# Optimization experiments

Measured on AMD Instinct MI355X. Metric: run time of the kernel, lower is better.

## Reference

```python
import jax, jax.numpy as jnp
import numpy as np

N_NODES = 100000
N_EDGES = 3200000
IN_C, HID_C, OUT_C = 128, 64, 64


def setup_inputs() -> dict:
    key = jax.random.key(0)
    k = jax.random.split(key, 6)
    x = jax.random.normal(k[0], (N_NODES, IN_C), dtype=jnp.float32)
    edge_index = jax.random.randint(k[1], (2, N_EDGES), 0, N_NODES, dtype=jnp.int64)
    edge_weight = jax.random.uniform(k[2], (N_EDGES,), dtype=jnp.float32)
    W1 = jax.random.normal(k[3], (IN_C, HID_C), dtype=jnp.float32) * (1.0 / np.sqrt(IN_C))
    b1 = jnp.zeros((HID_C,), dtype=jnp.float32)
    W2 = jax.random.normal(k[4], (HID_C, OUT_C), dtype=jnp.float32) * (1.0 / np.sqrt(HID_C))
    b2 = jnp.zeros((OUT_C,), dtype=jnp.float32)
    return {"x": x, "edge_index": edge_index, "edge_weight": edge_weight,
            "W1": W1, "b1": b1, "W2": W2, "b2": b2}


def _gcn_norm(edge_index, edge_weight, num_nodes, dtype):
    # PyG GCNConv default: add self-loops (weight 1), symmetric normalization
    loop = jnp.arange(num_nodes, dtype=edge_index.dtype)
    row = jnp.concatenate([edge_index[0], loop])  # sources
    col = jnp.concatenate([edge_index[1], loop])  # targets (aggregation dim)
    w = jnp.concatenate([edge_weight.astype(dtype), jnp.ones((num_nodes,), dtype)])
    deg = jax.ops.segment_sum(w, col, num_segments=num_nodes)
    deg_inv_sqrt = jnp.where(deg > 0, jax.lax.rsqrt(deg), jnp.zeros((), dtype))
    norm = deg_inv_sqrt[row] * w * deg_inv_sqrt[col]
    return row, col, norm


def _gcn_conv(h, row, col, norm, W, b, num_nodes):
    h = h @ W                      # [N, C_out]
    msg = h[row] * norm[:, None]   # gather over sources, scale by edge norm
    out = jax.ops.segment_sum(msg, col, num_segments=num_nodes)  # scatter-add to targets
    return out + b


def reference(x, edge_index, edge_weight, W1, b1, W2, b2):
    num_nodes = x.shape[0]
    row, col, norm = _gcn_norm(edge_index, edge_weight, num_nodes, x.dtype)
    h = _gcn_conv(x, row, col, norm, W1, b1, num_nodes)
    h = jax.nn.relu(h)
    return _gcn_conv(h, row, col, norm, W2, b2, num_nodes)
```

## Files before the change

kernel.cpp:

```cpp
#include <hip/hip_runtime.h>
#include <hip/hip_bf16.h>

#define N_NODES 100000
#define N_EDGES 3200000
#define IN_C 128
#define HID_C 64
#define OUT_C 64

#define NBUCKET 196
#define CH_GRID 1563
#define SC_EDGES 4096
#define SC_GRID 782

struct EdgeRec { int s; float v; };

__device__ __forceinline__ unsigned pack_bf16(float lo, float hi) {
    unsigned short l = __hip_bfloat16_raw(__float2bfloat16(lo)).x;
    unsigned short h = __hip_bfloat16_raw(__float2bfloat16(hi)).x;
    return ((unsigned)h << 16) | l;
}
__device__ __forceinline__ float bf_lo(unsigned u) {
    union { unsigned u; float f; } c; c.u = u << 16; return c.f;
}
__device__ __forceinline__ float bf_hi(unsigned u) {
    union { unsigned u; float f; } c; c.u = u & 0xffff0000u; return c.f;
}

__global__ __launch_bounds__(256) void coarse_hist(const int* __restrict__ tgt,
                                                   int* __restrict__ gcnt) {
    __shared__ int hist[256];
    int tid = threadIdx.x;
    hist[tid] = 0;
    __syncthreads();
    int base = blockIdx.x * 2048;
    for (int i = 0; i < 8; ++i) {
        int e = base + i * 256 + tid;
        if (e < N_EDGES) atomicAdd(&hist[tgt[e] >> 9], 1);
    }
    __syncthreads();
    if (hist[tid]) atomicAdd(&gcnt[tid], hist[tid]);
}

__global__ __launch_bounds__(256) void coarse_scan(const int* __restrict__ gcnt,
                                                   int* __restrict__ start,
                                                   int* __restrict__ cursor) {
    __shared__ int s[256];
    int tid = threadIdx.x;
    int v = gcnt[tid];
    s[tid] = v;
    __syncthreads();
    for (int off = 1; off < 256; off <<= 1) {
        int t = s[tid];
        int add = (tid >= off) ? s[tid - off] : 0;
        __syncthreads();
        s[tid] = t + add;
        __syncthreads();
    }
    int excl = s[tid] - v;
    start[tid] = excl;
    cursor[tid] = excl;
    if (tid == 255) start[256] = s[255];
}

__global__ __launch_bounds__(256) void scatter_coarse(const int* __restrict__ ei,
                                                      const float* __restrict__ ew,
                                                      int* __restrict__ gcursor,
                                                      uint2* __restrict__ tmp) {
    __shared__ int hist[256];
    __shared__ int scan[256];
    __shared__ int lcur[256];
    __shared__ int adj[256];
    __shared__ uint2 rec[SC_EDGES];
    __shared__ unsigned char bk[SC_EDGES];
    int tid = threadIdx.x;
    hist[tid] = 0;
    __syncthreads();
    int base = blockIdx.x * SC_EDGES;
    unsigned ys[16];
    float    ws[16];
    int      bs[16];
    for (int i = 0; i < 16; ++i) {
        int e = base + i * 256 + tid;
        if (e < N_EDGES) {
            int t = ei[N_EDGES + e];
            bs[i] = t >> 9;
            ys[i] = (unsigned)ei[e] | ((unsigned)(t & 511) << 17);
            ws[i] = ew[e];
            atomicAdd(&hist[bs[i]], 1);
        } else bs[i] = -1;
    }
    __syncthreads();
    int v = hist[tid];
    scan[tid] = v;
    __syncthreads();
    for (int off = 1; off < 256; off <<= 1) {
        int t = scan[tid];
        int add = (tid >= off) ? scan[tid - off] : 0;
        __syncthreads();
        scan[tid] = t + add;
        __syncthreads();
    }
    int excl = scan[tid] - v;
    int gb = (v > 0) ? atomicAdd(&gcursor[tid], v) : 0;
    lcur[tid] = excl;
    adj[tid] = gb - excl;
    __syncthreads();
    for (int i = 0; i < 16; ++i) {
        if (bs[i] >= 0) {
            int j = atomicAdd(&lcur[bs[i]], 1);
            rec[j] = make_uint2(__float_as_uint(ws[i]), ys[i]);
            bk[j] = (unsigned char)bs[i];
        }
    }
    __syncthreads();
    int count = N_EDGES - base;
    if (count > SC_EDGES) count = SC_EDGES;
    for (int j = tid; j < count; j += 256) {
        int b = bk[j];
        tmp[adj[b] + j] = rec[j];
    }
}

__global__ __launch_bounds__(512) void fine_sort(const int* __restrict__ start,
                                                 const uint2* __restrict__ tmp,
                                                 int* __restrict__ rowptr,
                                                 float* __restrict__ dis,
                                                 EdgeRec* __restrict__ ed) {
    __shared__ int   cnt[512];
    __shared__ float wdeg[512];
    __shared__ int   s[512];
    int tid = threadIdx.x;
    int nodeBase = blockIdx.x << 9;
    int bb = start[blockIdx.x];
    int be = start[blockIdx.x + 1];
    cnt[tid] = 0;
    wdeg[tid] = 0.f;
    __syncthreads();
    for (int e = bb + tid; e < be; e += 512) {
        uint2 r = tmp[e];
        int l = (r.y >> 17) & 511;
        atomicAdd(&cnt[l], 1);
        atomicAdd(&wdeg[l], __uint_as_float(r.x));
    }
    __syncthreads();
    int v = cnt[tid];
    s[tid] = v;
    __syncthreads();
    for (int off = 1; off < 512; off <<= 1) {
        int t = s[tid];
        int add = (tid >= off) ? s[tid - off] : 0;
        __syncthreads();
        s[tid] = t + add;
        __syncthreads();
    }
    int excl = s[tid] - v;
    int node = nodeBase + tid;
    if (node < N_NODES) {
        rowptr[node] = bb + excl;
        dis[node] = rsqrtf(wdeg[tid] + 1.0f);
    }
    if (node == N_NODES) rowptr[N_NODES] = N_EDGES;
    cnt[tid] = excl;
    __syncthreads();
    for (int e = bb + tid; e < be; e += 512) {
        uint2 r = tmp[e];
        int l = (r.y >> 17) & 511;
        int p = atomicAdd(&cnt[l], 1);
        EdgeRec o;
        o.s = (int)(r.y & 0x1FFFFu);
        o.v = __uint_as_float(r.x);
        ed[bb + p] = o;
    }
}

__global__ __launch_bounds__(256) void mm1_kernel(const float* __restrict__ x,
                                                  const float* __restrict__ W,
                                                  const float* __restrict__ dis,
                                                  unsigned* __restrict__ h) {
    __shared__ float xs[16][IN_C];
    __shared__ float wsm[IN_C][HID_C];
    int tid = threadIdx.x;
    {
        float4*       wd = (float4*)&wsm[0][0];
        const float4* wsrc = (const float4*)W;
        for (int i = tid; i < IN_C * HID_C / 4; i += 256) wd[i] = wsrc[i];
        float4*       xd = (float4*)&xs[0][0];
        const float4* xsrc = (const float4*)(x + (size_t)blockIdx.x * 16 * IN_C);
        for (int i = tid; i < 16 * IN_C / 4; i += 256) xd[i] = xsrc[i];
    }
    int rowBase = blockIdx.x * 16;
    __syncthreads();
    int c = tid & 63, rg = tid >> 6;
    float a0 = 0.f, a1 = 0.f, a2 = 0.f, a3 = 0.f;
    for (int k = 0; k < IN_C; ++k) {
        float wv = wsm[k][c];
        a0 += xs[rg * 4 + 0][k] * wv;
        a1 += xs[rg * 4 + 1][k] * wv;
        a2 += xs[rg * 4 + 2][k] * wv;
        a3 += xs[rg * 4 + 3][k] * wv;
    }
    a0 *= dis[rowBase + rg * 4 + 0];
    a1 *= dis[rowBase + rg * 4 + 1];
    a2 *= dis[rowBase + rg * 4 + 2];
    a3 *= dis[rowBase + rg * 4 + 3];
    float o0 = __shfl_xor(a0, 1, 64);
    float o1 = __shfl_xor(a1, 1, 64);
    float o2 = __shfl_xor(a2, 1, 64);
    float o3 = __shfl_xor(a3, 1, 64);
    if ((c & 1) == 0) {
        int ci = c >> 1;
        h[(rowBase + rg * 4 + 0) * 32 + ci] = pack_bf16(a0, o0);
        h[(rowBase + rg * 4 + 1) * 32 + ci] = pack_bf16(a1, o1);
        h[(rowBase + rg * 4 + 2) * 32 + ci] = pack_bf16(a2, o2);
        h[(rowBase + rg * 4 + 3) * 32 + ci] = pack_bf16(a3, o3);
    }
}

__global__ __launch_bounds__(256) void mm2_kernel(const float* __restrict__ a,
                                                  const float* __restrict__ W,
                                                  const float* __restrict__ dis,
                                                  unsigned* __restrict__ h) {
    __shared__ float as[16][HID_C];
    __shared__ float wsm[HID_C][OUT_C];
    int tid = threadIdx.x;
    {
        float4*       wd = (float4*)&wsm[0][0];
        const float4* wsrc = (const float4*)W;
        for (int i = tid; i < HID_C * OUT_C / 4; i += 256) wd[i] = wsrc[i];
        float4*       ad = (float4*)&as[0][0];
        const float4* asrc = (const float4*)(a + (size_t)blockIdx.x * 16 * HID_C);
        for (int i = tid; i < 16 * HID_C / 4; i += 256) ad[i] = asrc[i];
    }
    int rowBase = blockIdx.x * 16;
    __syncthreads();
    int c = tid & 63, rg = tid >> 6;
    float a0 = 0.f, a1 = 0.f, a2 = 0.f, a3 = 0.f;
    for (int k = 0; k < HID_C; ++k) {
        float wv = wsm[k][c];
        a0 += as[rg * 4 + 0][k] * wv;
        a1 += as[rg * 4 + 1][k] * wv;
        a2 += as[rg * 4 + 2][k] * wv;
        a3 += as[rg * 4 + 3][k] * wv;
    }
    a0 *= dis[rowBase + rg * 4 + 0];
    a1 *= dis[rowBase + rg * 4 + 1];
    a2 *= dis[rowBase + rg * 4 + 2];
    a3 *= dis[rowBase + rg * 4 + 3];
    float o0 = __shfl_xor(a0, 1, 64);
    float o1 = __shfl_xor(a1, 1, 64);
    float o2 = __shfl_xor(a2, 1, 64);
    float o3 = __shfl_xor(a3, 1, 64);
    if ((c & 1) == 0) {
        int ci = c >> 1;
        h[(rowBase + rg * 4 + 0) * 32 + ci] = pack_bf16(a0, o0);
        h[(rowBase + rg * 4 + 1) * 32 + ci] = pack_bf16(a1, o1);
        h[(rowBase + rg * 4 + 2) * 32 + ci] = pack_bf16(a2, o2);
        h[(rowBase + rg * 4 + 3) * 32 + ci] = pack_bf16(a3, o3);
    }
}

__global__ __launch_bounds__(256) void agg_kernel(const int* __restrict__ rowptr,
                                                  const EdgeRec* __restrict__ ed,
                                                  const unsigned* __restrict__ h,
                                                  const float* __restrict__ dis,
                                                  const float* __restrict__ b,
                                                  float* __restrict__ out,
                                                  int relu) {
    int node = blockIdx.x * 4 + (threadIdx.x >> 6);
    int lane = threadIdx.x & 63;
    int g = lane >> 3;
    int cl = lane & 7;
    int beg = rowptr[node];
    int end = rowptr[node + 1];
    const uint4* h16 = (const uint4*)h;
    float acc[8] = {0.f, 0.f, 0.f, 0.f, 0.f, 0.f, 0.f, 0.f};
    int e = beg + g;
    for (; e + 8 < end; e += 16) {
        EdgeRec r0 = ed[e];
        EdgeRec r1 = ed[e + 8];
        uint4 u0 = h16[r0.s * 8 + cl];
        uint4 u1 = h16[r1.s * 8 + cl];
        acc[0] += r0.v * bf_lo(u0.x); acc[1] += r0.v * bf_hi(u0.x);
        acc[2] += r0.v * bf_lo(u0.y); acc[3] += r0.v * bf_hi(u0.y);
        acc[4] += r0.v * bf_lo(u0.z); acc[5] += r0.v * bf_hi(u0.z);
        acc[6] += r0.v * bf_lo(u0.w); acc[7] += r0.v * bf_hi(u0.w);
        acc[0] += r1.v * bf_lo(u1.x); acc[1] += r1.v * bf_hi(u1.x);
        acc[2] += r1.v * bf_lo(u1.y); acc[3] += r1.v * bf_hi(u1.y);
        acc[4] += r1.v * bf_lo(u1.z); acc[5] += r1.v * bf_hi(u1.z);
        acc[6] += r1.v * bf_lo(u1.w); acc[7] += r1.v * bf_hi(u1.w);
    }
    if (e < end) {
        EdgeRec r0 = ed[e];
        uint4 u0 = h16[r0.s * 8 + cl];
        acc[0] += r0.v * bf_lo(u0.x); acc[1] += r0.v * bf_hi(u0.x);
        acc[2] += r0.v * bf_lo(u0.y); acc[3] += r0.v * bf_hi(u0.y);
        acc[4] += r0.v * bf_lo(u0.z); acc[5] += r0.v * bf_hi(u0.z);
        acc[6] += r0.v * bf_lo(u0.w); acc[7] += r0.v * bf_hi(u0.w);
    }
    #pragma unroll
    for (int k = 0; k < 8; ++k) {
        acc[k] += __shfl_xor(acc[k], 8, 64);
        acc[k] += __shfl_xor(acc[k], 16, 64);
        acc[k] += __shfl_xor(acc[k], 32, 64);
    }
    if (g == 0) {
        float d = dis[node];
        uint4 us = h16[node * 8 + cl];
        float hs[8] = { bf_lo(us.x), bf_hi(us.x), bf_lo(us.y), bf_hi(us.y),
                        bf_lo(us.z), bf_hi(us.z), bf_lo(us.w), bf_hi(us.w) };
        const float4* b4 = (const float4*)b;
        float4 bv0 = b4[cl * 2], bv1 = b4[cl * 2 + 1];
        float4 v0, v1;
        v0.x = d * (acc[0] + hs[0]) + bv0.x;
        v0.y = d * (acc[1] + hs[1]) + bv0.y;
        v0.z = d * (acc[2] + hs[2]) + bv0.z;
        v0.w = d * (acc[3] + hs[3]) + bv0.w;
        v1.x = d * (acc[4] + hs[4]) + bv1.x;
        v1.y = d * (acc[5] + hs[5]) + bv1.y;
        v1.z = d * (acc[6] + hs[6]) + bv1.z;
        v1.w = d * (acc[7] + hs[7]) + bv1.w;
        if (relu) {
            v0.x = fmaxf(v0.x, 0.f); v0.y = fmaxf(v0.y, 0.f);
            v0.z = fmaxf(v0.z, 0.f); v0.w = fmaxf(v0.w, 0.f);
            v1.x = fmaxf(v1.x, 0.f); v1.y = fmaxf(v1.y, 0.f);
            v1.z = fmaxf(v1.z, 0.f); v1.w = fmaxf(v1.w, 0.f);
        }
        float4* o4 = (float4*)out;
        o4[node * 16 + cl * 2]     = v0;
        o4[node * 16 + cl * 2 + 1] = v1;
    }
}

extern "C" void kernel_launch(void* const* d_in, const int* in_sizes, int n_in,
                              void* d_out, int out_size, void* d_ws, size_t ws_size,
                              hipStream_t stream) {
    const float* x  = (const float*)d_in[0];
    const int*   ei = (const int*)d_in[1];
    const float* ew = (const float*)d_in[2];
    const float* W1 = (const float*)d_in[3];
    const float* b1 = (const float*)d_in[4];
    const float* W2 = (const float*)d_in[5];
    const float* b2 = (const float*)d_in[6];
    float* out = (float*)d_out;

    char* p = (char*)d_ws;
    auto carve = [&](size_t bytes) { char* r = p; p += (bytes + 255) & ~(size_t)255; return r; };
    float*    dis     = (float*)carve(N_NODES * 4);
    int*      rowptr  = (int*)carve((N_NODES + 1) * 4);
    int*      gcnt    = (int*)carve(256 * 4);
    int*      start   = (int*)carve(257 * 4);
    int*      gcursor = (int*)carve(256 * 4);
    EdgeRec*  ed      = (EdgeRec*)carve((size_t)N_EDGES * 8);
    char*     r2      = carve((size_t)N_NODES * 64 * 2 + (size_t)N_NODES * 64 * 4);
    uint2*    tmp     = (uint2*)r2;
    unsigned* h       = (unsigned*)r2;
    float*    a       = (float*)(r2 + (size_t)N_NODES * 64 * 2);

    hipMemsetAsync(gcnt, 0, 256 * sizeof(int), stream);
    coarse_hist<<<CH_GRID, 256, 0, stream>>>(ei + N_EDGES, gcnt);
    coarse_scan<<<1, 256, 0, stream>>>(gcnt, start, gcursor);
    scatter_coarse<<<SC_GRID, 256, 0, stream>>>(ei, ew, gcursor, tmp);
    fine_sort<<<NBUCKET, 512, 0, stream>>>(start, tmp, rowptr, dis, ed);

    mm1_kernel<<<N_NODES / 16, 256, 0, stream>>>(x, W1, dis, h);
    agg_kernel<<<N_NODES / 4, 256, 0, stream>>>(rowptr, ed, h, dis, b1, a, 1);

    mm2_kernel<<<N_NODES / 16, 256, 0, stream>>>(a, W2, dis, h);
    agg_kernel<<<N_NODES / 4, 256, 0, stream>>>(rowptr, ed, h, dis, b2, out, 0);
}
```

Measured before the change: 418.2 us.

## Drop coarse histogram pass via padded buckets; vectorize matmuls; unroll aggregation

Removes the separate coarse histogram and scan kernels by scattering edges into fixed-capacity padded buckets (CAP per bucket) using atomic cursors, then scanning the final bucket counts afterward. This saves one full read of the target indices and two launches, but a bucket that exceeds CAP would overflow. The matmul kernels now read x/a rows as float4 from shared memory and use four weights per step. The aggregation loop gains a 4-edge unrolled body for more outstanding gathers.

```diff
diff --git a/kernel.cpp b/kernel.cpp
--- a/kernel.cpp
+++ b/kernel.cpp
@@ -8,9 +8,9 @@
 #define OUT_C 64
 
 #define NBUCKET 196
-#define CH_GRID 1563
 #define SC_EDGES 4096
 #define SC_GRID 782
+#define CAP 18432
 
 struct EdgeRec { int s; float v; };
 
@@ -24,42 +24,6 @@
 }
 __device__ __forceinline__ float bf_hi(unsigned u) {
     union { unsigned u; float f; } c; c.u = u & 0xffff0000u; return c.f;
-}
-
-__global__ __launch_bounds__(256) void coarse_hist(const int* __restrict__ tgt,
-                                                   int* __restrict__ gcnt) {
-    __shared__ int hist[256];
-    int tid = threadIdx.x;
-    hist[tid] = 0;
-    __syncthreads();
-    int base = blockIdx.x * 2048;
-    for (int i = 0; i < 8; ++i) {
-        int e = base + i * 256 + tid;
-        if (e < N_EDGES) atomicAdd(&hist[tgt[e] >> 9], 1);
-    }
-    __syncthreads();
-    if (hist[tid]) atomicAdd(&gcnt[tid], hist[tid]);
-}
-
-__global__ __launch_bounds__(256) void coarse_scan(const int* __restrict__ gcnt,
-                                                   int* __restrict__ start,
-                                                   int* __restrict__ cursor) {
-    __shared__ int s[256];
-    int tid = threadIdx.x;
-    int v = gcnt[tid];
-    s[tid] = v;
-    __syncthreads();
-    for (int off = 1; off < 256; off <<= 1) {
-        int t = s[tid];
-        int add = (tid >= off) ? s[tid - off] : 0;
-        __syncthreads();
-        s[tid] = t + add;
-        __syncthreads();
-    }
-    int excl = s[tid] - v;
-    start[tid] = excl;
-    cursor[tid] = excl;
-    if (tid == 255) start[256] = s[255];
 }
 
 __global__ __launch_bounds__(256) void scatter_coarse(const int* __restrict__ ei,
@@ -103,7 +67,7 @@
     int excl = scan[tid] - v;
     int gb = (v > 0) ? atomicAdd(&gcursor[tid], v) : 0;
     lcur[tid] = excl;
-    adj[tid] = gb - excl;
+    adj[tid] = tid * CAP + gb - excl;
     __syncthreads();
     for (int i = 0; i < 16; ++i) {
         if (bs[i] >= 0) {
@@ -121,8 +85,26 @@
     }
 }
 
+__global__ __launch_bounds__(256) void bucket_scan(const int* __restrict__ gcnt,
+                                                   int* __restrict__ start) {
+    __shared__ int s[256];
+    int tid = threadIdx.x;
+    int v = gcnt[tid];
+    s[tid] = v;
+    __syncthreads();
+    for (int off = 1; off < 256; off <<= 1) {
+        int t = s[tid];
+        int add = (tid >= off) ? s[tid - off] : 0;
+        __syncthreads();
+        s[tid] = t + add;
+        __syncthreads();
+    }
+    start[tid] = s[tid] - v;
+    if (tid == 255) start[256] = s[255];
+}
+
 __global__ __launch_bounds__(512) void fine_sort(const int* __restrict__ start,
-                                                 const uint2* __restrict__ tmp,
+                                                 const uint2* __restrict__ tmpPad,
                                                  int* __restrict__ rowptr,
                                                  float* __restrict__ dis,
                                                  EdgeRec* __restrict__ ed) {
@@ -132,12 +114,13 @@
     int tid = threadIdx.x;
     int nodeBase = blockIdx.x << 9;
     int bb = start[blockIdx.x];
-    int be = start[blockIdx.x + 1];
+    int nEdge = start[blockIdx.x + 1] - bb;
+    const uint2* tb = tmpPad + (size_t)blockIdx.x * CAP;
     cnt[tid] = 0;
     wdeg[tid] = 0.f;
     __syncthreads();
-    for (int e = bb + tid; e < be; e += 512) {
-        uint2 r = tmp[e];
+    for (int e = tid; e < nEdge; e += 512) {
+        uint2 r = tb[e];
         int l = (r.y >> 17) & 511;
         atomicAdd(&cnt[l], 1);
         atomicAdd(&wdeg[l], __uint_as_float(r.x));
@@ -162,8 +145,8 @@
     if (node == N_NODES) rowptr[N_NODES] = N_EDGES;
     cnt[tid] = excl;
     __syncthreads();
-    for (int e = bb + tid; e < be; e += 512) {
-        uint2 r = tmp[e];
+    for (int e = tid; e < nEdge; e += 512) {
+        uint2 r = tb[e];
         int l = (r.y >> 17) & 511;
         int p = atomicAdd(&cnt[l], 1);
         EdgeRec o;
@@ -177,8 +160,8 @@
                                                   const float* __restrict__ W,
                                                   const float* __restrict__ dis,
                                                   unsigned* __restrict__ h) {
-    __shared__ float xs[16][IN_C];
-    __shared__ float wsm[IN_C][HID_C];
+    __shared__ __align__(16) float xs[16][IN_C];
+    __shared__ __align__(16) float wsm[IN_C][HID_C];
     int tid = threadIdx.x;
     {
         float4*       wd = (float4*)&wsm[0][0];
@@ -191,13 +174,22 @@
     int rowBase = blockIdx.x * 16;
     __syncthreads();
     int c = tid & 63, rg = tid >> 6;
+    const float4* xr0 = (const float4*)&xs[rg * 4 + 0][0];
+    const float4* xr1 = (const float4*)&xs[rg * 4 + 1][0];
+    const float4* xr2 = (const float4*)&xs[rg * 4 + 2][0];
+    const float4* xr3 = (const float4*)&xs[rg * 4 + 3][0];
     float a0 = 0.f, a1 = 0.f, a2 = 0.f, a3 = 0.f;
-    for (int k = 0; k < IN_C; ++k) {
-        float wv = wsm[k][c];
-        a0 += xs[rg * 4 + 0][k] * wv;
-        a1 += xs[rg * 4 + 1][k] * wv;
-        a2 += xs[rg * 4 + 2][k] * wv;
-        a3 += xs[rg * 4 + 3][k] * wv;
+    #pragma unroll 4
+    for (int k4 = 0; k4 < IN_C / 4; ++k4) {
+        float4 x0 = xr0[k4], x1 = xr1[k4], x2 = xr2[k4], x3 = xr3[k4];
+        float w0 = wsm[4 * k4 + 0][c];
+        float w1 = wsm[4 * k4 + 1][c];
+        float w2 = wsm[4 * k4 + 2][c];
+        float w3 = wsm[4 * k4 + 3][c];
+        a0 += x0.x * w0 + x0.y * w1 + x0.z * w2 + x0.w * w3;
+        a1 += x1.x * w0 + x1.y * w1 + x1.z * w2 + x1.w * w3;
+        a2 += x2.x * w0 + x2.y * w1 + x2.z * w2 + x2.w * w3;
+        a3 += x3.x * w0 + x3.y * w1 + x3.z * w2 + x3.w * w3;
     }
     a0 *= dis[rowBase + rg * 4 + 0];
     a1 *= dis[rowBase + rg * 4 + 1];
@@ -220,8 +212,8 @@
                                                   const float* __restrict__ W,
                                                   const float* __restrict__ dis,
                                                   unsigned* __restrict__ h) {
-    __shared__ float as[16][HID_C];
-    __shared__ float wsm[HID_C][OUT_C];
+    __shared__ __align__(16) float as[16][HID_C];
+    __shared__ __align__(16) float wsm[HID_C][OUT_C];
     int tid = threadIdx.x;
     {
         float4*       wd = (float4*)&wsm[0][0];
@@ -234,13 +226,22 @@
     int rowBase = blockIdx.x * 16;
     __syncthreads();
     int c = tid & 63, rg = tid >> 6;
+    const float4* xr0 = (const float4*)&as[rg * 4 + 0][0];
+    const float4* xr1 = (const float4*)&as[rg * 4 + 1][0];
+    const float4* xr2 = (const float4*)&as[rg * 4 + 2][0];
+    const float4* xr3 = (const float4*)&as[rg * 4 + 3][0];
     float a0 = 0.f, a1 = 0.f, a2 = 0.f, a3 = 0.f;
-    for (int k = 0; k < HID_C; ++k) {
-        float wv = wsm[k][c];
-        a0 += as[rg * 4 + 0][k] * wv;
-        a1 += as[rg * 4 + 1][k] * wv;
-        a2 += as[rg * 4 + 2][k] * wv;
-        a3 += as[rg * 4 + 3][k] * wv;
+    #pragma unroll 4
+    for (int k4 = 0; k4 < HID_C / 4; ++k4) {
+        float4 x0 = xr0[k4], x1 = xr1[k4], x2 = xr2[k4], x3 = xr3[k4];
+        float w0 = wsm[4 * k4 + 0][c];
+        float w1 = wsm[4 * k4 + 1][c];
+        float w2 = wsm[4 * k4 + 2][c];
+        float w3 = wsm[4 * k4 + 3][c];
+        a0 += x0.x * w0 + x0.y * w1 + x0.z * w2 + x0.w * w3;
+        a1 += x1.x * w0 + x1.y * w1 + x1.z * w2 + x1.w * w3;
+        a2 += x2.x * w0 + x2.y * w1 + x2.z * w2 + x2.w * w3;
+        a3 += x3.x * w0 + x3.y * w1 + x3.z * w2 + x3.w * w3;
     }
     a0 *= dis[rowBase + rg * 4 + 0];
     a1 *= dis[rowBase + rg * 4 + 1];
@@ -275,6 +276,32 @@
     const uint4* h16 = (const uint4*)h;
     float acc[8] = {0.f, 0.f, 0.f, 0.f, 0.f, 0.f, 0.f, 0.f};
     int e = beg + g;
+    for (; e + 24 < end; e += 32) {
+        EdgeRec r0 = ed[e];
+        EdgeRec r1 = ed[e + 8];
+        EdgeRec r2 = ed[e + 16];
+        EdgeRec r3 = ed[e + 24];
+        uint4 u0 = h16[r0.s * 8 + cl];
+        uint4 u1 = h16[r1.s * 8 + cl];
+        uint4 u2 = h16[r2.s * 8 + cl];
+        uint4 u3 = h16[r3.s * 8 + cl];
+        acc[0] += r0.v * bf_lo(u0.x); acc[1] += r0.v * bf_hi(u0.x);
+        acc[2] += r0.v * bf_lo(u0.y); acc[3] += r0.v * bf_hi(u0.y);
+        acc[4] += r0.v * bf_lo(u0.z); acc[5] += r0.v * bf_hi(u0.z);
+        acc[6] += r0.v * bf_lo(u0.w); acc[7] += r0.v * bf_hi(u0.w);
+        acc[0] += r1.v * bf_lo(u1.x); acc[1] += r1.v * bf_hi(u1.x);
+        acc[2] += r1.v * bf_lo(u1.y); acc[3] += r1.v * bf_hi(u1.y);
+        acc[4] += r1.v * bf_lo(u1.z); acc[5] += r1.v * bf_hi(u1.z);
+        acc[6] += r1.v * bf_lo(u1.w); acc[7] += r1.v * bf_hi(u1.w);
+        acc[0] += r2.v * bf_lo(u2.x); acc[1] += r2.v * bf_hi(u2.x);
+        acc[2] += r2.v * bf_lo(u2.y); acc[3] += r2.v * bf_hi(u2.y);
+        acc[4] += r2.v * bf_lo(u2.z); acc[5] += r2.v * bf_hi(u2.z);
+        acc[6] += r2.v * bf_lo(u2.w); acc[7] += r2.v * bf_hi(u2.w);
+        acc[0] += r3.v * bf_lo(u3.x); acc[1] += r3.v * bf_hi(u3.x);
+        acc[2] += r3.v * bf_lo(u3.y); acc[3] += r3.v * bf_hi(u3.y);
+        acc[4] += r3.v * bf_lo(u3.z); acc[5] += r3.v * bf_hi(u3.z);
+        acc[6] += r3.v * bf_lo(u3.w); acc[7] += r3.v * bf_hi(u3.w);
+    }
     for (; e + 8 < end; e += 16) {
         EdgeRec r0 = ed[e];
         EdgeRec r1 = ed[e + 8];
@@ -347,20 +374,20 @@
     auto carve = [&](size_t bytes) { char* r = p; p += (bytes + 255) & ~(size_t)255; return r; };
     float*    dis     = (float*)carve(N_NODES * 4);
     int*      rowptr  = (int*)carve((N_NODES + 1) * 4);
-    int*      gcnt    = (int*)carve(256 * 4);
     int*      start   = (int*)carve(257 * 4);
     int*      gcursor = (int*)carve(256 * 4);
     EdgeRec*  ed      = (EdgeRec*)carve((size_t)N_EDGES * 8);
-    char*     r2      = carve((size_t)N_NODES * 64 * 2 + (size_t)N_NODES * 64 * 4);
-    uint2*    tmp     = (uint2*)r2;
+    size_t    r2sz    = (size_t)NBUCKET * CAP * 8;
+    size_t    hasz    = (size_t)N_NODES * 64 * 6;
+    char*     r2      = carve(r2sz > hasz ? r2sz : hasz);
+    uint2*    tmpPad  = (uint2*)r2;
     unsigned* h       = (unsigned*)r2;
     float*    a       = (float*)(r2 + (size_t)N_NODES * 64 * 2);
 
-    hipMemsetAsync(gcnt, 0, 256 * sizeof(int), stream);
-    coarse_hist<<<CH_GRID, 256, 0, stream>>>(ei + N_EDGES, gcnt);
-    coarse_scan<<<1, 256, 0, stream>>>(gcnt, start, gcursor);
-    scatter_coarse<<<SC_GRID, 256, 0, stream>>>(ei, ew, gcursor, tmp);
-    fine_sort<<<NBUCKET, 512, 0, stream>>>(start, tmp, rowptr, dis, ed);
+    hipMemsetAsync(gcursor, 0, 256 * sizeof(int), stream);
+    scatter_coarse<<<SC_GRID, 256, 0, stream>>>(ei, ew, gcursor, tmpPad);
+    bucket_scan<<<1, 256, 0, stream>>>(gcursor, start);
+    fine_sort<<<NBUCKET, 512, 0, stream>>>(start, tmpPad, rowptr, dis, ed);
 
     mm1_kernel<<<N_NODES / 16, 256, 0, stream>>>(x, W1, dis, h);
     agg_kernel<<<N_NODES / 4, 256, 0, stream>>>(rowptr, ed, h, dis, b1, a, 1);
```

Measured after the change: 392.1 us. 6.2% less time.
